# Performance work log

Measured on AMD Instinct MI355X. Metric: run time of the kernel, lower is better.

The kernel has to match this reference:

```python
import jax, jax.numpy as jnp
import numpy as np

D_MAX = 6.4
MASS = 40.0
GRAV = 9.8
N_PARTS = 4
B, NPTS, H, W = 512, 2048, 256, 256


def _interp(grid, xy):
    # grid: (B,H,W) over [-D_MAX,D_MAX]^2; xy: (B,N,2) -> (B,N,1) bilinear
    Bg, Hg, Wg = grid.shape
    gi = jnp.clip((xy[..., 0] + D_MAX) / (2.0 * D_MAX) * (Hg - 1), 0.0, Hg - 1.0)
    gj = jnp.clip((xy[..., 1] + D_MAX) / (2.0 * D_MAX) * (Wg - 1), 0.0, Wg - 1.0)
    i0 = jnp.clip(jnp.floor(gi).astype(jnp.int32), 0, Hg - 2)
    j0 = jnp.clip(jnp.floor(gj).astype(jnp.int32), 0, Wg - 2)
    wi = gi - i0.astype(grid.dtype)
    wj = gj - j0.astype(grid.dtype)
    flat = grid.reshape(Bg, Hg * Wg)
    gat = lambda ii, jj: jnp.take_along_axis(flat, ii * Wg + jj, axis=1)
    v = (gat(i0, j0) * (1 - wi) * (1 - wj) + gat(i0, j0 + 1) * (1 - wi) * wj
         + gat(i0 + 1, j0) * wi * (1 - wj) + gat(i0 + 1, j0 + 1) * wi * wj)
    return v[..., None]


def setup_inputs() -> dict:
    key = jax.random.key(0)
    ks = jax.random.split(key, 12)
    x = jax.random.uniform(ks[0], (B, 3), jnp.float32, -2.0, 2.0)
    xd = jax.random.normal(ks[1], (B, 3), jnp.float32)
    R, _ = jnp.linalg.qr(jax.random.normal(ks[2], (B, 3, 3), jnp.float32))
    omega = jax.random.normal(ks[3], (B, 3), jnp.float32) * 0.5
    A = jax.random.normal(ks[4], (B, 3, 3), jnp.float32) * 0.3
    I = jnp.einsum('bij,bkj->bik', A, A) + 2.0 * jnp.eye(3, dtype=jnp.float32)
    robot_points = jax.random.normal(ks[5], (B, NPTS, 3), jnp.float32) * 0.3
    z_grid = jax.random.normal(ks[6], (B, H, W), jnp.float32) * 0.1
    z_grid_grad = jax.random.normal(ks[7], (B, 2, H, W), jnp.float32) * 0.2
    stiffness = jax.random.uniform(ks[8], (B, H, W), jnp.float32, 500.0, 2000.0)
    damping = jax.random.uniform(ks[9], (B, H, W), jnp.float32, 10.0, 100.0)
    friction = jax.random.uniform(ks[10], (B, H, W), jnp.float32, 0.2, 1.0)
    driving_parts = jax.random.randint(ks[11], (NPTS,), 0, N_PARTS, jnp.int32)
    controls = jax.random.normal(jax.random.fold_in(key, 99), (B, N_PARTS), jnp.float32) * 2.0
    return dict(x=x, xd=xd, R=R, omega=omega, I=I, robot_points=robot_points,
                z_grid=z_grid, z_grid_grad=z_grid_grad, stiffness=stiffness,
                damping=damping, friction=friction, driving_parts=driving_parts,
                controls=controls)


def reference(x, xd, R, omega, I, robot_points, z_grid, z_grid_grad,
              stiffness, damping, friction, driving_parts, controls):
    n_pts = robot_points.shape[1]
    # local_to_global
    x_points = jnp.einsum('bij,bnj->bni', R, robot_points) + x[:, None]  # (B,N,3)
    xy = x_points[..., :2]
    z_points = _interp(z_grid, xy)              # (B,N,1)
    k_pts = _interp(stiffness, xy)
    d_pts = _interp(damping, xy)
    mu_pts = _interp(friction, xy)
    dh = x_points[..., 2:3] - z_points
    on_grid = ((x_points[..., 0:1] >= -D_MAX) & (x_points[..., 0:1] <= D_MAX)
               & (x_points[..., 1:2] >= -D_MAX) & (x_points[..., 1:2] <= D_MAX))
    in_contact = ((dh <= 0.0) & on_grid).astype(x.dtype)
    # surface normals from heightmap gradient: n = normalize([-dz/dx, -dz/dy, 1])
    gx = _interp(z_grid_grad[:, 0], xy)
    gy = _interp(z_grid_grad[:, 1], xy)
    n = jnp.concatenate([-gx, -gy, jnp.ones_like(gx)], axis=-1)
    n = n / jnp.linalg.norm(n, axis=-1, keepdims=True)
    # point velocities
    xd_points = xd[:, None] + jnp.cross(omega[:, None], x_points - x[:, None])
    xd_points_n = jnp.sum(xd_points * n, axis=-1, keepdims=True)
    F_spring = -(k_pts * dh + d_pts * xd_points_n) * n
    F_spring = F_spring * in_contact / n_pts
    thrust_dir = R[..., 0] / jnp.linalg.norm(R[..., 0], axis=-1, keepdims=True)
    Nmag = jnp.linalg.norm(F_spring, axis=2)  # (B,N)
    F_friction = jnp.zeros_like(F_spring)
    for i in range(N_PARTS):
        v_cmd = controls[:, i:i + 1] * thrust_dir          # (B,3)
        dv = v_cmd[:, None] - xd_points                     # (B,N,3)
        dv_n = jnp.sum(dv * n, axis=-1, keepdims=True)
        dv_tau = dv - dv_n * n
        Fi = mu_pts * Nmag[..., None] * jnp.tanh(dv_tau)
        mask = (driving_parts == i)[None, :, None]
        F_friction = jnp.where(mask, Fi, F_friction)
    torque = jnp.sum(jnp.cross(x_points - x[:, None], F_spring + F_friction), axis=1)
    I_inv = jnp.linalg.inv(I)
    omega_d = jnp.einsum('bij,bj->bi', I_inv, torque)
    F_grav = jnp.array([0.0, 0.0, -MASS * GRAV], dtype=x.dtype)
    F_cog = F_grav + F_spring.sum(axis=1) + F_friction.sum(axis=1)
    xdd = F_cog / MASS
    return (xd, xdd, omega_d, F_spring, F_friction)
```

## Files before the change

kernel.cpp:

```cpp
#include <hip/hip_runtime.h>

#pragma clang fp contract(off)

static constexpr int Bc    = 512;
static constexpr int NPTSc = 2048;
static constexpr int Hc    = 256;
static constexpr int Wc    = 256;
static constexpr float DMAXF = 6.4f;
static constexpr int CELLS = 2048;

__device__ __forceinline__ float bl(float g00, float g01, float g10, float g11,
                                    float wi, float wj) {
#pragma clang fp contract(off)
    return g00 * (1.0f - wi) * (1.0f - wj)
         + g01 * (1.0f - wi) * wj
         + g10 * wi * (1.0f - wj)
         + g11 * wi * wj;
}

__global__ __launch_bounds__(256)
void phys_points(const float* __restrict__ x, const float* __restrict__ xd,
                 const float* __restrict__ R, const float* __restrict__ omega,
                 const float* __restrict__ rp,
                 const float* __restrict__ zg, const float* __restrict__ zgg,
                 const float* __restrict__ kg, const float* __restrict__ dg,
                 const float* __restrict__ mug,
                 const int* __restrict__ dparts, const float* __restrict__ ctrl,
                 float* __restrict__ outFs, float* __restrict__ outFf,
                 float* __restrict__ partial)
{
#pragma clang fp contract(off)
    __shared__ float sg[6 * CELLS];
    __shared__ int sbox[4];

    const int tid = threadIdx.x;
    const int b = blockIdx.x >> 3;
    const int n = ((blockIdx.x & 7) << 8) + tid;

    float xb0 = x[b * 3 + 0], xb1 = x[b * 3 + 1], xb2 = x[b * 3 + 2];
    float xd0 = xd[b * 3 + 0], xd1 = xd[b * 3 + 1], xd2 = xd[b * 3 + 2];
    float om0 = omega[b * 3 + 0], om1 = omega[b * 3 + 1], om2 = omega[b * 3 + 2];
    float R00 = R[b * 9 + 0], R01 = R[b * 9 + 1], R02 = R[b * 9 + 2];
    float R10 = R[b * 9 + 3], R11 = R[b * 9 + 4], R12 = R[b * 9 + 5];
    float R20 = R[b * 9 + 6], R21 = R[b * 9 + 7], R22 = R[b * 9 + 8];

    const int part = dparts[n];
    const float cpart = ctrl[b * 4 + part];

    const int pbase = (b * NPTSc + n) * 3;
    float p0 = rp[pbase + 0], p1 = rp[pbase + 1], p2 = rp[pbase + 2];

    float xp0 = (R00 * p0 + R01 * p1 + R02 * p2) + xb0;
    float xp1 = (R10 * p0 + R11 * p1 + R12 * p2) + xb1;
    float xp2 = (R20 * p0 + R21 * p1 + R22 * p2) + xb2;

    float rx = xp0 - xb0, ry = xp1 - xb1, rz = xp2 - xb2;

    float gi = (xp0 + DMAXF) / (2.0f * DMAXF) * 255.0f;
    gi = fminf(fmaxf(gi, 0.0f), 255.0f);
    float gj = (xp1 + DMAXF) / (2.0f * DMAXF) * 255.0f;
    gj = fminf(fmaxf(gj, 0.0f), 255.0f);
    int i0 = (int)floorf(gi); i0 = min(max(i0, 0), Hc - 2);
    int j0 = (int)floorf(gj); j0 = min(max(j0, 0), Wc - 2);
    float wi = gi - (float)i0;
    float wj = gj - (float)j0;

    int mni = i0, mxi = i0, mnj = j0, mxj = j0;
    #pragma unroll
    for (int off = 32; off > 0; off >>= 1) {
        mni = min(mni, __shfl_xor(mni, off, 64));
        mxi = max(mxi, __shfl_xor(mxi, off, 64));
        mnj = min(mnj, __shfl_xor(mnj, off, 64));
        mxj = max(mxj, __shfl_xor(mxj, off, 64));
    }
    if (tid == 0) { sbox[0] = 255; sbox[1] = 0; sbox[2] = 255; sbox[3] = 0; }
    __syncthreads();
    if ((tid & 63) == 0) {
        atomicMin(&sbox[0], mni); atomicMax(&sbox[1], mxi);
        atomicMin(&sbox[2], mnj); atomicMax(&sbox[3], mxj);
    }
    __syncthreads();
    const int bmin_i = sbox[0], bmin_j = sbox[2];
    const int ih = sbox[1] - bmin_i + 2;
    const int jw = sbox[3] - bmin_j + 2;
    const bool use_lds = (ih * jw) <= CELLS;

    const int gb  = b * (Hc * Wc);
    const int gb2 = b * (2 * Hc * Wc);
    const float* planes[6] = { zg + gb, kg + gb, dg + gb, mug + gb,
                               zgg + gb2, zgg + gb2 + Hc * Wc };

    float cv[6][4];
    if (use_lds) {
        const int tx = tid & 63, ty = tid >> 6;
        #pragma unroll
        for (int p = 0; p < 6; ++p) {
            const float* src = planes[p] + bmin_i * Wc + bmin_j;
            float* dst = sg + p * CELLS;
            for (int r = ty; r < ih; r += 4)
                for (int c = tx; c < jw; c += 64)
                    dst[r * jw + c] = src[r * Wc + c];
        }
        __syncthreads();
        const int la = (i0 - bmin_i) * jw + (j0 - bmin_j);
        #pragma unroll
        for (int p = 0; p < 6; ++p) {
            const float* s = sg + p * CELLS + la;
            cv[p][0] = s[0]; cv[p][1] = s[1];
            cv[p][2] = s[jw]; cv[p][3] = s[jw + 1];
        }
    } else {
        const int la = i0 * Wc + j0;
        #pragma unroll
        for (int p = 0; p < 6; ++p) {
            const float* s = planes[p] + la;
            cv[p][0] = s[0]; cv[p][1] = s[1];
            cv[p][2] = s[Wc]; cv[p][3] = s[Wc + 1];
        }
    }

    float zp  = bl(cv[0][0], cv[0][1], cv[0][2], cv[0][3], wi, wj);
    float kp  = bl(cv[1][0], cv[1][1], cv[1][2], cv[1][3], wi, wj);
    float dpv = bl(cv[2][0], cv[2][1], cv[2][2], cv[2][3], wi, wj);
    float mup = bl(cv[3][0], cv[3][1], cv[3][2], cv[3][3], wi, wj);
    float gx  = bl(cv[4][0], cv[4][1], cv[4][2], cv[4][3], wi, wj);
    float gy  = bl(cv[5][0], cv[5][1], cv[5][2], cv[5][3], wi, wj);

    float dh = xp2 - zp;
    bool on_grid = (xp0 >= -DMAXF) && (xp0 <= DMAXF) &&
                   (xp1 >= -DMAXF) && (xp1 <= DMAXF);
    float contact = ((dh <= 0.0f) && on_grid) ? 1.0f : 0.0f;

    float nx = -gx, ny = -gy, nz = 1.0f;
    float nn = sqrtf(nx * nx + ny * ny + nz * nz);
    nx /= nn; ny /= nn; nz /= nn;

    float vx = xd0 + (om1 * rz - om2 * ry);
    float vy = xd1 + (om2 * rx - om0 * rz);
    float vz = xd2 + (om0 * ry - om1 * rx);

    float xdn = vx * nx + vy * ny + vz * nz;
    float s = -(kp * dh + dpv * xdn);
    const float scale = contact * (1.0f / 2048.0f);
    float Fs0 = (s * nx) * scale;
    float Fs1 = (s * ny) * scale;
    float Fs2 = (s * nz) * scale;

    float Nmag = sqrtf(Fs0 * Fs0 + Fs1 * Fs1 + Fs2 * Fs2);

    float t0 = R00, t1 = R10, t2 = R20;
    float tn = sqrtf(t0 * t0 + t1 * t1 + t2 * t2);
    t0 /= tn; t1 /= tn; t2 /= tn;

    float dv0 = cpart * t0 - vx;
    float dv1 = cpart * t1 - vy;
    float dv2 = cpart * t2 - vz;
    float dvn = dv0 * nx + dv1 * ny + dv2 * nz;
    float dt0 = dv0 - dvn * nx;
    float dt1 = dv1 - dvn * ny;
    float dt2 = dv2 - dvn * nz;
    float mN = mup * Nmag;
    float Ff0 = mN * tanhf(dt0);
    float Ff1 = mN * tanhf(dt1);
    float Ff2 = mN * tanhf(dt2);

    outFs[pbase + 0] = Fs0;
    outFs[pbase + 1] = Fs1;
    outFs[pbase + 2] = Fs2;
    outFf[pbase + 0] = Ff0;
    outFf[pbase + 1] = Ff1;
    outFf[pbase + 2] = Ff2;

    float Ft0 = Fs0 + Ff0, Ft1 = Fs1 + Ff1, Ft2 = Fs2 + Ff2;
    float vals[9];
    vals[0] = ry * Ft2 - rz * Ft1;
    vals[1] = rz * Ft0 - rx * Ft2;
    vals[2] = rx * Ft1 - ry * Ft0;
    vals[3] = Fs0; vals[4] = Fs1; vals[5] = Fs2;
    vals[6] = Ff0; vals[7] = Ff1; vals[8] = Ff2;

    #pragma unroll
    for (int k = 0; k < 9; ++k) {
        float v = vals[k];
        #pragma unroll
        for (int off = 32; off > 0; off >>= 1)
            v += __shfl_xor(v, off, 64);
        vals[k] = v;
    }
    if ((tid & 63) == 0) {
        const int widx = ((blockIdx.x & 7) << 2) + (tid >> 6);
        float* pb = partial + ((size_t)(b * 32 + widx)) * 9;
        #pragma unroll
        for (int k = 0; k < 9; ++k) pb[k] = vals[k];
    }
}

__global__ __launch_bounds__(64)
void phys_final(const float* __restrict__ xd, const float* __restrict__ Imat,
                const float* __restrict__ partial,
                float* __restrict__ out_xd, float* __restrict__ out_xdd,
                float* __restrict__ out_omd)
{
#pragma clang fp contract(off)
    const int b = blockIdx.x;
    const int lane = threadIdx.x;

    float v[9];
    if (lane < 32) {
        const float* pb = partial + ((size_t)(b * 32 + lane)) * 9;
        #pragma unroll
        for (int k = 0; k < 9; ++k) v[k] = pb[k];
    } else {
        #pragma unroll
        for (int k = 0; k < 9; ++k) v[k] = 0.0f;
    }
    #pragma unroll
    for (int k = 0; k < 9; ++k) {
        float t = v[k];
        #pragma unroll
        for (int off = 32; off > 0; off >>= 1)
            t += __shfl_xor(t, off, 64);
        v[k] = t;
    }

    if (lane == 0) {
        float tq0 = v[0], tq1 = v[1], tq2 = v[2];
        float sFs0 = v[3], sFs1 = v[4], sFs2 = v[5];
        float sFf0 = v[6], sFf1 = v[7], sFf2 = v[8];

        float a00 = Imat[b * 9 + 0], a01 = Imat[b * 9 + 1], a02 = Imat[b * 9 + 2];
        float a10 = Imat[b * 9 + 3], a11 = Imat[b * 9 + 4], a12 = Imat[b * 9 + 5];
        float a20 = Imat[b * 9 + 6], a21 = Imat[b * 9 + 7], a22 = Imat[b * 9 + 8];

        float c00 = a11 * a22 - a12 * a21;
        float c01 = a02 * a21 - a01 * a22;
        float c02 = a01 * a12 - a02 * a11;
        float c10 = a12 * a20 - a10 * a22;
        float c11 = a00 * a22 - a02 * a20;
        float c12 = a02 * a10 - a00 * a12;
        float c20 = a10 * a21 - a11 * a20;
        float c21 = a01 * a20 - a00 * a21;
        float c22 = a00 * a11 - a01 * a10;
        float det = a00 * c00 + a01 * c10 + a02 * c20;
        float id = 1.0f / det;

        float od0 = (c00 * tq0 + c01 * tq1 + c02 * tq2) * id;
        float od1 = (c10 * tq0 + c11 * tq1 + c12 * tq2) * id;
        float od2 = (c20 * tq0 + c21 * tq1 + c22 * tq2) * id;

        float fc0 = (0.0f + sFs0) + sFf0;
        float fc1 = (0.0f + sFs1) + sFf1;
        float fc2 = (-40.0f * 9.8f + sFs2) + sFf2;
        float xdd0 = fc0 / 40.0f, xdd1 = fc1 / 40.0f, xdd2 = fc2 / 40.0f;

        out_xd[b * 3 + 0] = xd[b * 3 + 0];
        out_xd[b * 3 + 1] = xd[b * 3 + 1];
        out_xd[b * 3 + 2] = xd[b * 3 + 2];
        out_xdd[b * 3 + 0] = xdd0;
        out_xdd[b * 3 + 1] = xdd1;
        out_xdd[b * 3 + 2] = xdd2;
        out_omd[b * 3 + 0] = od0;
        out_omd[b * 3 + 1] = od1;
        out_omd[b * 3 + 2] = od2;
    }
}

extern "C" void kernel_launch(void* const* d_in, const int* in_sizes, int n_in,
                              void* d_out, int out_size, void* d_ws, size_t ws_size,
                              hipStream_t stream)
{
    const float* x    = (const float*)d_in[0];
    const float* xd   = (const float*)d_in[1];
    const float* R    = (const float*)d_in[2];
    const float* om   = (const float*)d_in[3];
    const float* Imat = (const float*)d_in[4];
    const float* rp   = (const float*)d_in[5];
    const float* zg   = (const float*)d_in[6];
    const float* zgg  = (const float*)d_in[7];
    const float* kg   = (const float*)d_in[8];
    const float* dg   = (const float*)d_in[9];
    const float* mug  = (const float*)d_in[10];
    const int* dparts = (const int*)d_in[11];
    const float* ctrl = (const float*)d_in[12];

    float* out = (float*)d_out;
    const int B3 = Bc * 3;
    float* out_xd  = out;
    float* out_xdd = out + B3;
    float* out_omd = out + 2 * B3;
    float* outFs   = out + 3 * B3;
    float* outFf   = out + 3 * B3 + (size_t)Bc * NPTSc * 3;

    float* partial = (float*)d_ws;

    phys_points<<<Bc * NPTSc / 256, 256, 0, stream>>>(
        x, xd, R, om, rp, zg, zgg, kg, dg, mug, dparts, ctrl, outFs, outFf, partial);
    phys_final<<<Bc, 64, 0, stream>>>(
        xd, Imat, partial, out_xd, out_xdd, out_omd);
}
```

Before: 693.5 us.

## Fuse point and final kernels into one block-per-batch kernel with vectorized LDS staging

Merges the two kernels into one kernel that runs one 512-thread block per batch element, with each thread handling four points. The grid window is staged into LDS once per batch using float4 loads into a fixed 52x64 tile, and the final reduction and inverse-inertia solve happen in the same block. This removes the second launch and the partial-sum round trip, and replaces per-8-block redundant window loads with a single load. It also swaps tanhf and the normal normalization for fast exp2/rcp/rsq intrinsics, which may change numerics slightly. The fixed tile is smaller than before, so wider point spreads fall back to global gathers.

```diff
diff --git a/kernel.cpp b/kernel.cpp
--- a/kernel.cpp
+++ b/kernel.cpp
@@ -7,35 +7,37 @@
 static constexpr int Hc    = 256;
 static constexpr int Wc    = 256;
 static constexpr float DMAXF = 6.4f;
-static constexpr int CELLS = 2048;
-
-__device__ __forceinline__ float bl(float g00, float g01, float g10, float g11,
-                                    float wi, float wj) {
-#pragma clang fp contract(off)
-    return g00 * (1.0f - wi) * (1.0f - wj)
-         + g01 * (1.0f - wi) * wj
-         + g10 * wi * (1.0f - wj)
-         + g11 * wi * wj;
+static constexpr int WROWS = 52;
+static constexpr int WCOLS = 64;
+static constexpr int CELLS = WROWS * WCOLS;
+static constexpr int PPT   = 4;
+
+__device__ __forceinline__ float ftanh(float v) {
+    float e = __builtin_amdgcn_exp2f(fabsf(v) * 2.885390082f);
+    float r = 1.0f - 2.0f * __builtin_amdgcn_rcpf(e + 1.0f);
+    return copysignf(r, v);
 }
 
-__global__ __launch_bounds__(256)
-void phys_points(const float* __restrict__ x, const float* __restrict__ xd,
-                 const float* __restrict__ R, const float* __restrict__ omega,
-                 const float* __restrict__ rp,
-                 const float* __restrict__ zg, const float* __restrict__ zgg,
-                 const float* __restrict__ kg, const float* __restrict__ dg,
-                 const float* __restrict__ mug,
-                 const int* __restrict__ dparts, const float* __restrict__ ctrl,
-                 float* __restrict__ outFs, float* __restrict__ outFf,
-                 float* __restrict__ partial)
+__global__ __launch_bounds__(512, 4)
+void phys_all(const float* __restrict__ x, const float* __restrict__ xd,
+              const float* __restrict__ R, const float* __restrict__ omega,
+              const float* __restrict__ Imat,
+              const float* __restrict__ rp,
+              const float* __restrict__ zg, const float* __restrict__ zgg,
+              const float* __restrict__ kg, const float* __restrict__ dg,
+              const float* __restrict__ mug,
+              const int* __restrict__ dparts, const float* __restrict__ ctrl,
+              float* __restrict__ outFs, float* __restrict__ outFf,
+              float* __restrict__ out_xd, float* __restrict__ out_xdd,
+              float* __restrict__ out_omd)
 {
 #pragma clang fp contract(off)
     __shared__ float sg[6 * CELLS];
     __shared__ int sbox[4];
+    __shared__ float red[8 * 9];
 
     const int tid = threadIdx.x;
-    const int b = blockIdx.x >> 3;
-    const int n = ((blockIdx.x & 7) << 8) + tid;
+    const int b = blockIdx.x;
 
     float xb0 = x[b * 3 + 0], xb1 = x[b * 3 + 1], xb2 = x[b * 3 + 2];
     float xd0 = xd[b * 3 + 0], xd1 = xd[b * 3 + 1], xd2 = xd[b * 3 + 2];
@@ -44,28 +46,41 @@
     float R10 = R[b * 9 + 3], R11 = R[b * 9 + 4], R12 = R[b * 9 + 5];
     float R20 = R[b * 9 + 6], R21 = R[b * 9 + 7], R22 = R[b * 9 + 8];
 
-    const int part = dparts[n];
-    const float cpart = ctrl[b * 4 + part];
-
-    const int pbase = (b * NPTSc + n) * 3;
-    float p0 = rp[pbase + 0], p1 = rp[pbase + 1], p2 = rp[pbase + 2];
-
-    float xp0 = (R00 * p0 + R01 * p1 + R02 * p2) + xb0;
-    float xp1 = (R10 * p0 + R11 * p1 + R12 * p2) + xb1;
-    float xp2 = (R20 * p0 + R21 * p1 + R22 * p2) + xb2;
-
-    float rx = xp0 - xb0, ry = xp1 - xb1, rz = xp2 - xb2;
-
-    float gi = (xp0 + DMAXF) / (2.0f * DMAXF) * 255.0f;
-    gi = fminf(fmaxf(gi, 0.0f), 255.0f);
-    float gj = (xp1 + DMAXF) / (2.0f * DMAXF) * 255.0f;
-    gj = fminf(fmaxf(gj, 0.0f), 255.0f);
-    int i0 = (int)floorf(gi); i0 = min(max(i0, 0), Hc - 2);
-    int j0 = (int)floorf(gj); j0 = min(max(j0, 0), Wc - 2);
-    float wi = gi - (float)i0;
-    float wj = gj - (float)j0;
-
-    int mni = i0, mxi = i0, mnj = j0, mxj = j0;
+    float t0 = R00, t1 = R10, t2 = R20;
+    float tn = sqrtf(t0 * t0 + t1 * t1 + t2 * t2);
+    t0 /= tn; t1 /= tn; t2 /= tn;
+
+    float xpA[PPT][3];
+    float wiA[PPT], wjA[PPT], cpA[PPT];
+    int pkA[PPT];
+    int mni = 255, mxi = 0, mnj = 255, mxj = 0;
+    #pragma unroll
+    for (int k = 0; k < PPT; ++k) {
+        const int n = tid + (k << 9);
+        const int pb3 = (b * NPTSc + n) * 3;
+        float p0 = rp[pb3 + 0], p1 = rp[pb3 + 1], p2 = rp[pb3 + 2];
+        cpA[k] = ctrl[b * 4 + dparts[n]];
+
+        float xp0 = (R00 * p0 + R01 * p1 + R02 * p2) + xb0;
+        float xp1 = (R10 * p0 + R11 * p1 + R12 * p2) + xb1;
+        float xp2 = (R20 * p0 + R21 * p1 + R22 * p2) + xb2;
+        xpA[k][0] = xp0; xpA[k][1] = xp1; xpA[k][2] = xp2;
+
+        float gi = (xp0 + DMAXF) / (2.0f * DMAXF) * 255.0f;
+        gi = fminf(fmaxf(gi, 0.0f), 255.0f);
+        float gj = (xp1 + DMAXF) / (2.0f * DMAXF) * 255.0f;
+        gj = fminf(fmaxf(gj, 0.0f), 255.0f);
+        int i0 = (int)floorf(gi); i0 = min(max(i0, 0), Hc - 2);
+        int j0 = (int)floorf(gj); j0 = min(max(j0, 0), Wc - 2);
+        wiA[k] = gi - (float)i0;
+        wjA[k] = gj - (float)j0;
+        bool og = (xp0 >= -DMAXF) && (xp0 <= DMAXF) &&
+                  (xp1 >= -DMAXF) && (xp1 <= DMAXF);
+        pkA[k] = i0 | (j0 << 8) | (og ? (1 << 16) : 0);
+        mni = min(mni, i0); mxi = max(mxi, i0);
+        mnj = min(mnj, j0); mxj = max(mxj, j0);
+    }
+
     #pragma unroll
     for (int off = 32; off > 0; off >>= 1) {
         mni = min(mni, __shfl_xor(mni, off, 64));
@@ -80,153 +95,158 @@
         atomicMin(&sbox[2], mnj); atomicMax(&sbox[3], mxj);
     }
     __syncthreads();
-    const int bmin_i = sbox[0], bmin_j = sbox[2];
-    const int ih = sbox[1] - bmin_i + 2;
-    const int jw = sbox[3] - bmin_j + 2;
-    const bool use_lds = (ih * jw) <= CELLS;
+    const int bi = sbox[0];
+    const int bj = sbox[2] & ~3;
+    const int ih = sbox[1] - bi + 2;
+    const int jw = sbox[3] - bj + 2;
+    const bool use_lds = (ih <= WROWS) && (jw <= WCOLS);
 
     const int gb  = b * (Hc * Wc);
     const int gb2 = b * (2 * Hc * Wc);
     const float* planes[6] = { zg + gb, kg + gb, dg + gb, mug + gb,
                                zgg + gb2, zgg + gb2 + Hc * Wc };
 
-    float cv[6][4];
     if (use_lds) {
-        const int tx = tid & 63, ty = tid >> 6;
-        #pragma unroll
-        for (int p = 0; p < 6; ++p) {
-            const float* src = planes[p] + bmin_i * Wc + bmin_j;
-            float* dst = sg + p * CELLS;
-            for (int r = ty; r < ih; r += 4)
-                for (int c = tx; c < jw; c += 64)
-                    dst[r * jw + c] = src[r * Wc + c];
+        const int w = tid >> 6, l = tid & 63;
+        const int rsub = l >> 4;
+        const int csub = (l & 15) << 2;
+        const int jcol = min(bj + csub, Wc - 4);
+        const int ngrp = (ih + 3) >> 2;
+        for (int g = w; g < ngrp; g += 8) {
+            const int r = (g << 2) + rsub;
+            const int grow = min(bi + r, Hc - 1);
+            #pragma unroll
+            for (int p = 0; p < 6; ++p) {
+                const float4 v = *reinterpret_cast<const float4*>(
+                    planes[p] + grow * Wc + jcol);
+                *reinterpret_cast<float4*>(&sg[p * CELLS + r * WCOLS + csub]) = v;
+            }
         }
         __syncthreads();
-        const int la = (i0 - bmin_i) * jw + (j0 - bmin_j);
-        #pragma unroll
-        for (int p = 0; p < 6; ++p) {
-            const float* s = sg + p * CELLS + la;
-            cv[p][0] = s[0]; cv[p][1] = s[1];
-            cv[p][2] = s[jw]; cv[p][3] = s[jw + 1];
+    }
+
+    float vsum[9];
+    #pragma unroll
+    for (int c = 0; c < 9; ++c) vsum[c] = 0.0f;
+
+    #pragma unroll
+    for (int k = 0; k < PPT; ++k) {
+        const int n = tid + (k << 9);
+        const int pb3 = (b * NPTSc + n) * 3;
+        const int i0 = pkA[k] & 255;
+        const int j0 = (pkA[k] >> 8) & 255;
+        const bool og = (pkA[k] >> 16) & 1;
+        const float wi = wiA[k], wj = wjA[k];
+
+        float cv[6][4];
+        if (use_lds) {
+            const int la = (i0 - bi) * WCOLS + (j0 - bj);
+            #pragma unroll
+            for (int p = 0; p < 6; ++p) {
+                const float* s = sg + p * CELLS + la;
+                cv[p][0] = s[0];     cv[p][1] = s[1];
+                cv[p][2] = s[WCOLS]; cv[p][3] = s[WCOLS + 1];
+            }
+        } else {
+            const int la = i0 * Wc + j0;
+            #pragma unroll
+            for (int p = 0; p < 6; ++p) {
+                const float* s = planes[p] + la;
+                cv[p][0] = s[0];  cv[p][1] = s[1];
+                cv[p][2] = s[Wc]; cv[p][3] = s[Wc + 1];
+            }
         }
-    } else {
-        const int la = i0 * Wc + j0;
-        #pragma unroll
-        for (int p = 0; p < 6; ++p) {
-            const float* s = planes[p] + la;
-            cv[p][0] = s[0]; cv[p][1] = s[1];
-            cv[p][2] = s[Wc]; cv[p][3] = s[Wc + 1];
-        }
-    }
-
-    float zp  = bl(cv[0][0], cv[0][1], cv[0][2], cv[0][3], wi, wj);
-    float kp  = bl(cv[1][0], cv[1][1], cv[1][2], cv[1][3], wi, wj);
-    float dpv = bl(cv[2][0], cv[2][1], cv[2][2], cv[2][3], wi, wj);
-    float mup = bl(cv[3][0], cv[3][1], cv[3][2], cv[3][3], wi, wj);
-    float gx  = bl(cv[4][0], cv[4][1], cv[4][2], cv[4][3], wi, wj);
-    float gy  = bl(cv[5][0], cv[5][1], cv[5][2], cv[5][3], wi, wj);
-
-    float dh = xp2 - zp;
-    bool on_grid = (xp0 >= -DMAXF) && (xp0 <= DMAXF) &&
-                   (xp1 >= -DMAXF) && (xp1 <= DMAXF);
-    float contact = ((dh <= 0.0f) && on_grid) ? 1.0f : 0.0f;
-
-    float nx = -gx, ny = -gy, nz = 1.0f;
-    float nn = sqrtf(nx * nx + ny * ny + nz * nz);
-    nx /= nn; ny /= nn; nz /= nn;
-
-    float vx = xd0 + (om1 * rz - om2 * ry);
-    float vy = xd1 + (om2 * rx - om0 * rz);
-    float vz = xd2 + (om0 * ry - om1 * rx);
-
-    float xdn = vx * nx + vy * ny + vz * nz;
-    float s = -(kp * dh + dpv * xdn);
-    const float scale = contact * (1.0f / 2048.0f);
-    float Fs0 = (s * nx) * scale;
-    float Fs1 = (s * ny) * scale;
-    float Fs2 = (s * nz) * scale;
-
-    float Nmag = sqrtf(Fs0 * Fs0 + Fs1 * Fs1 + Fs2 * Fs2);
-
-    float t0 = R00, t1 = R10, t2 = R20;
-    float tn = sqrtf(t0 * t0 + t1 * t1 + t2 * t2);
-    t0 /= tn; t1 /= tn; t2 /= tn;
-
-    float dv0 = cpart * t0 - vx;
-    float dv1 = cpart * t1 - vy;
-    float dv2 = cpart * t2 - vz;
-    float dvn = dv0 * nx + dv1 * ny + dv2 * nz;
-    float dt0 = dv0 - dvn * nx;
-    float dt1 = dv1 - dvn * ny;
-    float dt2 = dv2 - dvn * nz;
-    float mN = mup * Nmag;
-    float Ff0 = mN * tanhf(dt0);
-    float Ff1 = mN * tanhf(dt1);
-    float Ff2 = mN * tanhf(dt2);
-
-    outFs[pbase + 0] = Fs0;
-    outFs[pbase + 1] = Fs1;
-    outFs[pbase + 2] = Fs2;
-    outFf[pbase + 0] = Ff0;
-    outFf[pbase + 1] = Ff1;
-    outFf[pbase + 2] = Ff2;
-
-    float Ft0 = Fs0 + Ff0, Ft1 = Fs1 + Ff1, Ft2 = Fs2 + Ff2;
-    float vals[9];
-    vals[0] = ry * Ft2 - rz * Ft1;
-    vals[1] = rz * Ft0 - rx * Ft2;
-    vals[2] = rx * Ft1 - ry * Ft0;
-    vals[3] = Fs0; vals[4] = Fs1; vals[5] = Fs2;
-    vals[6] = Ff0; vals[7] = Ff1; vals[8] = Ff2;
-
-    #pragma unroll
-    for (int k = 0; k < 9; ++k) {
-        float v = vals[k];
+
+        const float omwi = 1.0f - wi, omwj = 1.0f - wj;
+        float zp = cv[0][0] * omwi * omwj + cv[0][1] * omwi * wj
+                 + cv[0][2] * wi * omwj   + cv[0][3] * wi * wj;
+        const float w00 = omwi * omwj, w01 = omwi * wj;
+        const float w10 = wi * omwj,   w11 = wi * wj;
+        float kp  = cv[1][0]*w00 + cv[1][1]*w01 + cv[1][2]*w10 + cv[1][3]*w11;
+        float dpv = cv[2][0]*w00 + cv[2][1]*w01 + cv[2][2]*w10 + cv[2][3]*w11;
+        float mup = cv[3][0]*w00 + cv[3][1]*w01 + cv[3][2]*w10 + cv[3][3]*w11;
+        float gx  = cv[4][0]*w00 + cv[4][1]*w01 + cv[4][2]*w10 + cv[4][3]*w11;
+        float gy  = cv[5][0]*w00 + cv[5][1]*w01 + cv[5][2]*w10 + cv[5][3]*w11;
+
+        const float xp0 = xpA[k][0], xp1 = xpA[k][1], xp2 = xpA[k][2];
+        const float rx = xp0 - xb0, ry = xp1 - xb1, rz = xp2 - xb2;
+
+        float dh = xp2 - zp;
+        float contact = ((dh <= 0.0f) && og) ? 1.0f : 0.0f;
+
+        float nx = -gx, ny = -gy;
+        float invn = __builtin_amdgcn_rsqf(nx * nx + ny * ny + 1.0f);
+        nx *= invn; ny *= invn;
+        const float nz = invn;
+
+        float vx = xd0 + (om1 * rz - om2 * ry);
+        float vy = xd1 + (om2 * rx - om0 * rz);
+        float vz = xd2 + (om0 * ry - om1 * rx);
+
+        float xdn = vx * nx + vy * ny + vz * nz;
+        float s = -(kp * dh + dpv * xdn);
+        const float scale = contact * (1.0f / 2048.0f);
+        float Fs0 = (s * nx) * scale;
+        float Fs1 = (s * ny) * scale;
+        float Fs2 = (s * nz) * scale;
+
+        float Nmag = sqrtf(Fs0 * Fs0 + Fs1 * Fs1 + Fs2 * Fs2);
+
+        const float cp = cpA[k];
+        float dv0 = cp * t0 - vx;
+        float dv1 = cp * t1 - vy;
+        float dv2 = cp * t2 - vz;
+        float dvn = dv0 * nx + dv1 * ny + dv2 * nz;
+        float dt0 = dv0 - dvn * nx;
+        float dt1 = dv1 - dvn * ny;
+        float dt2 = dv2 - dvn * nz;
+        float mN = mup * Nmag;
+        float Ff0 = mN * ftanh(dt0);
+        float Ff1 = mN * ftanh(dt1);
+        float Ff2 = mN * ftanh(dt2);
+
+        outFs[pb3 + 0] = Fs0;
+        outFs[pb3 + 1] = Fs1;
+        outFs[pb3 + 2] = Fs2;
+        outFf[pb3 + 0] = Ff0;
+        outFf[pb3 + 1] = Ff1;
+        outFf[pb3 + 2] = Ff2;
+
+        float Ft0 = Fs0 + Ff0, Ft1 = Fs1 + Ff1, Ft2 = Fs2 + Ff2;
+        vsum[0] += ry * Ft2 - rz * Ft1;
+        vsum[1] += rz * Ft0 - rx * Ft2;
+        vsum[2] += rx * Ft1 - ry * Ft0;
+        vsum[3] += Fs0; vsum[4] += Fs1; vsum[5] += Fs2;
+        vsum[6] += Ff0; vsum[7] += Ff1; vsum[8] += Ff2;
+    }
+
+    #pragma unroll
+    for (int c = 0; c < 9; ++c) {
+        float v = vsum[c];
         #pragma unroll
         for (int off = 32; off > 0; off >>= 1)
             v += __shfl_xor(v, off, 64);
-        vals[k] = v;
+        vsum[c] = v;
     }
     if ((tid & 63) == 0) {
-        const int widx = ((blockIdx.x & 7) << 2) + (tid >> 6);
-        float* pb = partial + ((size_t)(b * 32 + widx)) * 9;
+        const int w = tid >> 6;
         #pragma unroll
-        for (int k = 0; k < 9; ++k) pb[k] = vals[k];
-    }
-}
-
-__global__ __launch_bounds__(64)
-void phys_final(const float* __restrict__ xd, const float* __restrict__ Imat,
-                const float* __restrict__ partial,
-                float* __restrict__ out_xd, float* __restrict__ out_xdd,
-                float* __restrict__ out_omd)
-{
-#pragma clang fp contract(off)
-    const int b = blockIdx.x;
-    const int lane = threadIdx.x;
-
-    float v[9];
-    if (lane < 32) {
-        const float* pb = partial + ((size_t)(b * 32 + lane)) * 9;
+        for (int c = 0; c < 9; ++c) red[w * 9 + c] = vsum[c];
+    }
+    __syncthreads();
+
+    if (tid == 0) {
+        float sum[9];
         #pragma unroll
-        for (int k = 0; k < 9; ++k) v[k] = pb[k];
-    } else {
-        #pragma unroll
-        for (int k = 0; k < 9; ++k) v[k] = 0.0f;
-    }
-    #pragma unroll
-    for (int k = 0; k < 9; ++k) {
-        float t = v[k];
-        #pragma unroll
-        for (int off = 32; off > 0; off >>= 1)
-            t += __shfl_xor(t, off, 64);
-        v[k] = t;
-    }
-
-    if (lane == 0) {
-        float tq0 = v[0], tq1 = v[1], tq2 = v[2];
-        float sFs0 = v[3], sFs1 = v[4], sFs2 = v[5];
-        float sFf0 = v[6], sFf1 = v[7], sFf2 = v[8];
+        for (int c = 0; c < 9; ++c) {
+            float s = red[c];
+            #pragma unroll
+            for (int w = 1; w < 8; ++w) s += red[w * 9 + c];
+            sum[c] = s;
+        }
+        float tq0 = sum[0], tq1 = sum[1], tq2 = sum[2];
+        float sFs0 = sum[3], sFs1 = sum[4], sFs2 = sum[5];
+        float sFf0 = sum[6], sFf1 = sum[7], sFf2 = sum[8];
 
         float a00 = Imat[b * 9 + 0], a01 = Imat[b * 9 + 1], a02 = Imat[b * 9 + 2];
         float a10 = Imat[b * 9 + 3], a11 = Imat[b * 9 + 4], a12 = Imat[b * 9 + 5];
@@ -251,14 +271,13 @@
         float fc0 = (0.0f + sFs0) + sFf0;
         float fc1 = (0.0f + sFs1) + sFf1;
         float fc2 = (-40.0f * 9.8f + sFs2) + sFf2;
-        float xdd0 = fc0 / 40.0f, xdd1 = fc1 / 40.0f, xdd2 = fc2 / 40.0f;
-
-        out_xd[b * 3 + 0] = xd[b * 3 + 0];
-        out_xd[b * 3 + 1] = xd[b * 3 + 1];
-        out_xd[b * 3 + 2] = xd[b * 3 + 2];
-        out_xdd[b * 3 + 0] = xdd0;
-        out_xdd[b * 3 + 1] = xdd1;
-        out_xdd[b * 3 + 2] = xdd2;
+
+        out_xd[b * 3 + 0] = xd0;
+        out_xd[b * 3 + 1] = xd1;
+        out_xd[b * 3 + 2] = xd2;
+        out_xdd[b * 3 + 0] = fc0 / 40.0f;
+        out_xdd[b * 3 + 1] = fc1 / 40.0f;
+        out_xdd[b * 3 + 2] = fc2 / 40.0f;
         out_omd[b * 3 + 0] = od0;
         out_omd[b * 3 + 1] = od1;
         out_omd[b * 3 + 2] = od2;
@@ -291,10 +310,7 @@
     float* outFs   = out + 3 * B3;
     float* outFf   = out + 3 * B3 + (size_t)Bc * NPTSc * 3;
 
-    float* partial = (float*)d_ws;
-
-    phys_points<<<Bc * NPTSc / 256, 256, 0, stream>>>(
-        x, xd, R, om, rp, zg, zgg, kg, dg, mug, dparts, ctrl, outFs, outFf, partial);
-    phys_final<<<Bc, 64, 0, stream>>>(
-        xd, Imat, partial, out_xd, out_xdd, out_omd);
+    phys_all<<<Bc, 512, 0, stream>>>(
+        x, xd, R, om, Imat, rp, zg, zgg, kg, dg, mug, dparts, ctrl,
+        outFs, outFf, out_xd, out_xdd, out_omd);
 }
```

New measurement: 557.7 us. 1.24x faster.
